# Performance work log

Hardware: AMD Instinct MI355X
Metric: run time of the kernel (lower is better)

The kernel has to match this reference:

```python
import jax, jax.numpy as jnp
import numpy as np

N_HEADS = 16

def _rotate_half(t):
    # t: [B, H, T, hs]; split last dim in half, return cat(-x2, x1)
    hs = t.shape[-1]
    x1, x2 = t[..., : hs // 2], t[..., hs // 2 :]
    return jnp.concatenate((-x2, x1), axis=-1)

def _rope_pos(T, hs, dtype):
    inv_freq = 1.0 / (10000.0 ** (jnp.arange(0, hs, 2, dtype=jnp.float32) / hs))
    freqs = jnp.arange(T, dtype=jnp.float32)[:, None] * inv_freq[None, :]  # [T, hs/2]
    pos = jnp.concatenate((freqs, freqs), axis=-1)  # [T, hs]
    return pos

def setup_inputs() -> dict:
    key = jax.random.key(0)
    ks = jax.random.split(key, 5)
    d = 2048
    x = jax.random.normal(ks[0], (2, 2048, d), dtype=jnp.float32)
    W_attn = jax.random.normal(ks[1], (d, 3 * d), dtype=jnp.float32) * (1.0 / np.sqrt(d))
    b_attn = jax.random.normal(ks[2], (3 * d,), dtype=jnp.float32) * 0.02
    W_proj = jax.random.normal(ks[3], (d, d), dtype=jnp.float32) * (1.0 / np.sqrt(d))
    b_proj = jax.random.normal(ks[4], (d,), dtype=jnp.float32) * 0.02
    return {"x": x, "W_attn": W_attn, "b_attn": b_attn, "W_proj": W_proj, "b_proj": b_proj}

def reference(x, W_attn, b_attn, W_proj, b_proj):
    B, T, C = x.shape
    nh = N_HEADS
    hs = C // nh
    qkv = x @ W_attn + b_attn  # [B, T, 3C]
    q, k, v = jnp.split(qkv, 3, axis=-1)
    # [B, T, C] -> [B, nh, T, hs]
    def to_heads(t):
        return t.reshape(B, T, nh, hs).transpose(0, 2, 1, 3)
    q, k, v = to_heads(q), to_heads(k), to_heads(v)
    # RoPE
    pos = _rope_pos(T, hs, x.dtype)  # [T, hs]
    cos, sin = jnp.cos(pos).astype(x.dtype), jnp.sin(pos).astype(x.dtype)
    q = q * cos + _rotate_half(q) * sin
    k = k * cos + _rotate_half(k) * sin
    # causal SDPA
    scale = 1.0 / np.sqrt(hs)
    scores = jnp.einsum('bhqd,bhkd->bhqk', q, k) * scale  # [B, nh, T, T]
    causal = jnp.tril(jnp.ones((T, T), dtype=bool))
    scores = jnp.where(causal, scores, jnp.finfo(scores.dtype).min)
    att = jax.nn.softmax(scores, axis=-1)
    out = jnp.einsum('bhqk,bhkd->bhqd', att, v)  # [B, nh, T, hs]
    y = out.transpose(0, 2, 1, 3).reshape(B, T, C)
    return y @ W_proj + b_proj
```

## Files before the change

### kernel.cpp

```cpp
#include <hip/hip_runtime.h>
#include <stdint.h>

typedef unsigned short u16;
typedef __attribute__((ext_vector_type(8))) short short8;
typedef __attribute__((ext_vector_type(4))) float f32x4;
typedef __attribute__((ext_vector_type(4))) unsigned short u16x4;

#define DEV __device__ __forceinline__

DEV u16 f2bf(float f) {
  union { float f; unsigned u; } v; v.f = f;
  unsigned r = v.u + 0x7fffu + ((v.u >> 16) & 1u);
  return (u16)(r >> 16);
}
DEV float bf2f(u16 b) {
  union { unsigned u; float f; } v; v.u = ((unsigned)b) << 16;
  return v.f;
}
DEV void gload_lds16(const void* g, void* l) {
  __builtin_amdgcn_global_load_lds((const __attribute__((address_space(1))) void*)g,
                                   (__attribute__((address_space(3))) void*)l,
                                   16, 0, 0);
}
DEV void block_barrier() {
  asm volatile("" ::: "memory");
  __builtin_amdgcn_s_barrier();
  asm volatile("" ::: "memory");
}

__global__ void k_conv(const float* __restrict__ in, u16* __restrict__ out, int n4) {
  int i = blockIdx.x * blockDim.x + threadIdx.x;
  if (i >= n4) return;
  const f32x4 v = *(const f32x4*)(in + (size_t)i * 4);
  u16x4 o;
  o[0] = f2bf(v[0]); o[1] = f2bf(v[1]); o[2] = f2bf(v[2]); o[3] = f2bf(v[3]);
  *(u16x4*)(out + (size_t)i * 4) = o;
}

__global__ void k_tconv(const float* __restrict__ in, u16* __restrict__ out, int R, int C) {
  __shared__ float tile[32][33];
  int c0 = blockIdx.x * 32, r0 = blockIdx.y * 32;
  int tx = threadIdx.x, ty = threadIdx.y;
#pragma unroll
  for (int j = 0; j < 32; j += 8)
    tile[ty + j][tx] = in[(size_t)(r0 + ty + j) * C + (c0 + tx)];
  __syncthreads();
#pragma unroll
  for (int j = 0; j < 32; j += 8)
    out[(size_t)(c0 + ty + j) * R + (r0 + tx)] = f2bf(tile[tx][ty + j]);
}

__global__ void k_rope(const u16* __restrict__ qkv, u16* __restrict__ qh, u16* __restrict__ kh) {
  int m = blockIdx.x;
  int t = m & 2047, b = m >> 11;
  int tid = threadIdx.x;
  int h = blockIdx.y * 4 + (tid >> 6);
  int j = tid & 63;
  float inv = expf((float)j * -0.14391156831212787f);
  float ang = (float)t * inv;
  float s, c;
  sincosf(ang, &s, &c);
  size_t ibase = (size_t)m * 6144 + (size_t)h * 128;
  size_t obase = ((size_t)(b * 16 + h) * 2048 + t) * 128;
  float q1 = bf2f(qkv[ibase + j]),        q2 = bf2f(qkv[ibase + 64 + j]);
  qh[obase + j]      = f2bf(q1 * c - q2 * s);
  qh[obase + 64 + j] = f2bf(q2 * c + q1 * s);
  float k1 = bf2f(qkv[ibase + 2048 + j]), k2 = bf2f(qkv[ibase + 2048 + 64 + j]);
  kh[obase + j]      = f2bf(k1 * c - k2 * s);
  kh[obase + 64 + j] = f2bf(k2 * c + k1 * s);
}

__global__ void k_vtrans(const u16* __restrict__ qkv, u16* __restrict__ vt) {
  __shared__ u16 tile[32][33];
  int bh = blockIdx.z;
  int b = bh >> 4, h = bh & 15;
  int t0 = blockIdx.x * 32, d0 = blockIdx.y * 32;
  int tx = threadIdx.x, ty = threadIdx.y;
#pragma unroll
  for (int j = 0; j < 32; j += 8)
    tile[ty + j][tx] = qkv[(size_t)(b * 2048 + t0 + ty + j) * 6144 + 4096 + h * 128 + d0 + tx];
  __syncthreads();
#pragma unroll
  for (int j = 0; j < 32; j += 8)
    vt[((size_t)bh * 128 + d0 + ty + j) * 2048 + (t0 + tx)] = tile[tx][ty + j];
}

template <bool OUT_BF16>
__global__ __launch_bounds__(256) void k_gemm_tn(const u16* __restrict__ A,
                                                 const u16* __restrict__ Bt,
                                                 const float* __restrict__ bias,
                                                 void* __restrict__ Cv,
                                                 int M, int N, int K) {
  __shared__ __align__(16) short lA[128 * 64];
  __shared__ __align__(16) short lB[128 * 64];
  const int tid = threadIdx.x;
  const int wid = tid >> 6, lane = tid & 63;
  const int bm = blockIdx.x * 128, bn = blockIdx.y * 128;
  const int wm = (wid >> 1) * 64, wn = (wid & 1) * 64;
  const int r = lane & 15, kq = lane >> 4;

  f32x4 acc[4][4];
  const f32x4 zero = {0.f, 0.f, 0.f, 0.f};
#pragma unroll
  for (int i = 0; i < 4; ++i)
#pragma unroll
    for (int j = 0; j < 4; ++j) acc[i][j] = zero;

  for (int k0 = 0; k0 < K; k0 += 64) {
#pragma unroll
    for (int i = 0; i < 4; ++i) {
      int c = (wid * 4 + i) * 64 + lane;
      int row = c >> 3, cb = c & 7;
      gload_lds16(A + (size_t)(bm + row) * K + k0 + cb * 8, (char*)lA + (wid * 4 + i) * 1024);
      gload_lds16(Bt + (size_t)(bn + row) * K + k0 + cb * 8, (char*)lB + (wid * 4 + i) * 1024);
    }
    asm volatile("s_waitcnt vmcnt(0)" ::: "memory");
    __syncthreads();
#pragma unroll
    for (int kk = 0; kk < 2; ++kk) {
      short8 af[4], bfr[4];
#pragma unroll
      for (int mf = 0; mf < 4; ++mf)
        af[mf] = *(const short8*)&lA[(wm + mf * 16 + r) * 64 + kk * 32 + kq * 8];
#pragma unroll
      for (int nf = 0; nf < 4; ++nf)
        bfr[nf] = *(const short8*)&lB[(wn + nf * 16 + r) * 64 + kk * 32 + kq * 8];
#pragma unroll
      for (int mf = 0; mf < 4; ++mf)
#pragma unroll
        for (int nf = 0; nf < 4; ++nf)
          acc[mf][nf] = __builtin_amdgcn_mfma_f32_16x16x32_bf16(af[mf], bfr[nf], acc[mf][nf], 0, 0, 0);
    }
    __syncthreads();
  }
#pragma unroll
  for (int mf = 0; mf < 4; ++mf)
#pragma unroll
    for (int nf = 0; nf < 4; ++nf) {
      int n = bn + wn + nf * 16 + r;
      float bv = bias[n];
#pragma unroll
      for (int i = 0; i < 4; ++i) {
        int m = bm + wm + mf * 16 + kq * 4 + i;
        float val = acc[mf][nf][i] + bv;
        if (OUT_BF16)
          ((u16*)Cv)[(size_t)m * N + n] = f2bf(val);
        else
          ((float*)Cv)[(size_t)m * N + n] = val;
      }
    }
}

__global__ __launch_bounds__(256) void k_attn(const u16* __restrict__ qh,
                                              const u16* __restrict__ kh,
                                              const u16* __restrict__ vt,
                                              u16* __restrict__ out) {
  __shared__ __align__(16) short lK[2][64 * 128];
  __shared__ __align__(16) short lV[2][128 * 64];
  __shared__ __align__(16) short lP[64 * 64];
  const int tid = threadIdx.x, wid = tid >> 6, lane = tid & 63;
  const int p = blockIdx.x, h = blockIdx.y, b = blockIdx.z;
  const size_t bh = (size_t)b * 16 + h;
  const u16* qb = qh + bh * 2048 * 128;
  const u16* kb = kh + bh * 2048 * 128;
  const u16* vb = vt + bh * 128 * 2048;
  const int r = lane & 15, kq = lane >> 4;
  const int r7 = r & 7;
  const int wrow = wid * 16;
  const float scale2 = 0.08838834764831845f * 1.4426950408889634f;

  int koff[4], voff[4];
#pragma unroll
  for (int i = 0; i < 4; ++i) {
    int ci = (wid * 4 + i) * 64 + lane;
    int krow = ci >> 4, kch = ci & 15;
    koff[i] = krow * 128 + ((kch ^ (krow & 7)) * 8);
    int vrow = ci >> 3, vch = ci & 7;
    voff[i] = vrow * 2048 + ((vch ^ (vrow & 7)) * 8);
  }

#pragma unroll 1
  for (int seg = 0; seg < 2; ++seg) {
    const int j = seg ? 31 - p : p;
    const int q0 = j * 64;
    const int nkt = j + 1;

    short8 qa[4];
#pragma unroll
    for (int kk = 0; kk < 4; ++kk)
      qa[kk] = *(const short8*)(qb + (size_t)(q0 + wrow + r) * 128 + kk * 32 + kq * 8);

    f32x4 O[8];
    const f32x4 zero = {0.f, 0.f, 0.f, 0.f};
#pragma unroll
    for (int nf = 0; nf < 8; ++nf) O[nf] = zero;
    float m_run[4], l_run[4];
#pragma unroll
    for (int i = 0; i < 4; ++i) { m_run[i] = -1e30f; l_run[i] = 0.f; }

#pragma unroll
    for (int i = 0; i < 4; ++i) {
      gload_lds16(kb + koff[i], (char*)&lK[0][0] + (wid * 4 + i) * 1024);
      gload_lds16(vb + voff[i], (char*)&lV[0][0] + (wid * 4 + i) * 1024);
    }

#pragma unroll 1
    for (int kt = 0; kt < nkt; ++kt) {
      const int cur = kt & 1;
      if (kt + 1 < nkt) {
        const size_t kbase = (size_t)(kt + 1) * 8192, vbase = (size_t)(kt + 1) * 64;
#pragma unroll
        for (int i = 0; i < 4; ++i) {
          gload_lds16(kb + kbase + koff[i], (char*)&lK[cur ^ 1][0] + (wid * 4 + i) * 1024);
          gload_lds16(vb + vbase + voff[i], (char*)&lV[cur ^ 1][0] + (wid * 4 + i) * 1024);
        }
        asm volatile("s_waitcnt vmcnt(8)" ::: "memory");
      } else {
        asm volatile("s_waitcnt vmcnt(0)" ::: "memory");
      }
      block_barrier();

      f32x4 S[4];
#pragma unroll
      for (int nf = 0; nf < 4; ++nf) S[nf] = zero;
#pragma unroll
      for (int kk = 0; kk < 4; ++kk) {
        short8 kf[4];
#pragma unroll
        for (int nf = 0; nf < 4; ++nf)
          kf[nf] = *(const short8*)&lK[cur][(nf * 16 + r) * 128 + ((kk * 4 + kq) ^ r7) * 8];
#pragma unroll
        for (int nf = 0; nf < 4; ++nf)
          S[nf] = __builtin_amdgcn_mfma_f32_16x16x32_bf16(qa[kk], kf[nf], S[nf], 0, 0, 0);
      }

      float mnew[4];
#pragma unroll
      for (int i = 0; i < 4; ++i) mnew[i] = m_run[i];
      if (kt == nkt - 1) {
#pragma unroll
        for (int nf = 0; nf < 4; ++nf)
#pragma unroll
          for (int i = 0; i < 4; ++i) {
            float s = S[nf][i] * scale2;
            int kg = kt * 64 + nf * 16 + r;
            int qg = q0 + wrow + kq * 4 + i;
            s = (kg > qg) ? -1e30f : s;
            S[nf][i] = s;
            mnew[i] = fmaxf(mnew[i], s);
          }
      } else {
#pragma unroll
        for (int nf = 0; nf < 4; ++nf)
#pragma unroll
          for (int i = 0; i < 4; ++i) {
            float s = S[nf][i] * scale2;
            S[nf][i] = s;
            mnew[i] = fmaxf(mnew[i], s);
          }
      }
#pragma unroll
      for (int i = 0; i < 4; ++i) {
        float v = mnew[i];
        v = fmaxf(v, __shfl_xor(v, 1));
        v = fmaxf(v, __shfl_xor(v, 2));
        v = fmaxf(v, __shfl_xor(v, 4));
        v = fmaxf(v, __shfl_xor(v, 8));
        mnew[i] = v;
      }
      float rs[4];
#pragma unroll
      for (int i = 0; i < 4; ++i) {
        rs[i] = exp2f(m_run[i] - mnew[i]);
        l_run[i] *= rs[i];
        m_run[i] = mnew[i];
      }
#pragma unroll
      for (int nf = 0; nf < 8; ++nf)
#pragma unroll
        for (int i = 0; i < 4; ++i) O[nf][i] *= rs[i];

      {
        float lsum[4] = {0.f, 0.f, 0.f, 0.f};
#pragma unroll
        for (int nf = 0; nf < 4; ++nf)
#pragma unroll
          for (int i = 0; i < 4; ++i) {
            float pv = exp2f(S[nf][i] - m_run[i]);
            lsum[i] += pv;
            int row = wrow + kq * 4 + i;
            int cl = (nf * 2 + (r >> 3)) ^ ((kq * 4 + i) & 7);
            lP[row * 64 + cl * 8 + r7] = (short)f2bf(pv);
          }
#pragma unroll
        for (int i = 0; i < 4; ++i) {
          float v = lsum[i];
          v += __shfl_xor(v, 1);
          v += __shfl_xor(v, 2);
          v += __shfl_xor(v, 4);
          v += __shfl_xor(v, 8);
          l_run[i] += v;
        }
      }

#pragma unroll
      for (int kk = 0; kk < 2; ++kk) {
        short8 pa = *(const short8*)&lP[(wrow + r) * 64 + ((kk * 4 + kq) ^ r7) * 8];
#pragma unroll
        for (int nf = 0; nf < 8; ++nf) {
          short8 vf = *(const short8*)&lV[cur][(nf * 16 + r) * 64 + ((kk * 4 + kq) ^ r7) * 8];
          O[nf] = __builtin_amdgcn_mfma_f32_16x16x32_bf16(pa, vf, O[nf], 0, 0, 0);
        }
      }
      asm volatile("s_waitcnt lgkmcnt(0)" ::: "memory");
      block_barrier();
    }

    float inv[4];
#pragma unroll
    for (int i = 0; i < 4; ++i) inv[i] = 1.f / l_run[i];
#pragma unroll
    for (int nf = 0; nf < 8; ++nf)
#pragma unroll
      for (int i = 0; i < 4; ++i) {
        int qg = q0 + wrow + kq * 4 + i;
        out[(size_t)(b * 2048 + qg) * 2048 + h * 128 + nf * 16 + r] = f2bf(O[nf][i] * inv[i]);
      }
  }
}

extern "C" void kernel_launch(void* const* d_in, const int* in_sizes, int n_in,
                              void* d_out, int out_size, void* d_ws, size_t ws_size,
                              hipStream_t stream) {
  const float* x      = (const float*)d_in[0];
  const float* W_attn = (const float*)d_in[1];
  const float* b_attn = (const float*)d_in[2];
  const float* W_proj = (const float*)d_in[3];
  const float* b_proj = (const float*)d_in[4];
  float* y = (float*)d_out;

  u16* xb     = (u16*)d_ws;
  u16* wqkvT  = xb     + (size_t)4096 * 2048;
  u16* wprojT = wqkvT  + (size_t)6144 * 2048;
  u16* qkv    = wprojT + (size_t)2048 * 2048;
  u16* qh     = qkv    + (size_t)4096 * 6144;
  u16* kh     = qh     + (size_t)4096 * 2048;
  u16* vt     = kh     + (size_t)4096 * 2048;
  u16* attout = vt     + (size_t)4096 * 2048;
  if (ws_size < (size_t)83886080 * 2) return;

  k_conv<<<8192, 256, 0, stream>>>(x, xb, 2097152);
  k_tconv<<<dim3(192, 64), dim3(32, 8), 0, stream>>>(W_attn, wqkvT, 2048, 6144);
  k_tconv<<<dim3(64, 64), dim3(32, 8), 0, stream>>>(W_proj, wprojT, 2048, 2048);
  k_gemm_tn<true><<<dim3(32, 48), 256, 0, stream>>>(xb, wqkvT, b_attn, qkv, 4096, 6144, 2048);
  k_rope<<<dim3(4096, 4), 256, 0, stream>>>(qkv, qh, kh);
  k_vtrans<<<dim3(64, 4, 32), dim3(32, 8), 0, stream>>>(qkv, vt);
  k_attn<<<dim3(16, 16, 2), 256, 0, stream>>>(qh, kh, vt, attout);
  k_gemm_tn<false><<<dim3(32, 16), 256, 0, stream>>>(attout, wprojT, b_proj, y, 4096, 2048, 2048);
}
```

Before: 348.3 us.

## Double-buffer GEMM tiles with XOR-swizzled LDS and 128x256 block tiles

Replaces the single-buffered 128x128 GEMM with a 512-thread 128x256 tile kernel that prefetches the next K-tile into a second LDS buffer while computing the current one. It applies an XOR swizzle to LDS chunk placement to avoid bank conflicts and raises wave priority around the MFMA block. The goal is to hide global-load latency and cut LDS conflicts in both projection GEMMs. It uses 96KB of LDS per block, which limits occupancy, and adds an extra barrier per iteration.

```diff
diff --git a/kernel.cpp b/kernel.cpp
--- a/kernel.cpp
+++ b/kernel.cpp
@@ -86,18 +86,35 @@
 }
 
 template <bool OUT_BF16>
-__global__ __launch_bounds__(256) void k_gemm_tn(const u16* __restrict__ A,
-                                                 const u16* __restrict__ Bt,
-                                                 const float* __restrict__ bias,
-                                                 void* __restrict__ Cv,
-                                                 int M, int N, int K) {
-  __shared__ __align__(16) short lA[128 * 64];
-  __shared__ __align__(16) short lB[128 * 64];
+__global__ __launch_bounds__(512, 2) void k_gemm2(const u16* __restrict__ A,
+                                                  const u16* __restrict__ Bt,
+                                                  const float* __restrict__ bias,
+                                                  void* __restrict__ Cv,
+                                                  int M, int N, int K) {
+  __shared__ __align__(16) short lA[2][128 * 64];
+  __shared__ __align__(16) short lB[2][256 * 64];
   const int tid = threadIdx.x;
   const int wid = tid >> 6, lane = tid & 63;
-  const int bm = blockIdx.x * 128, bn = blockIdx.y * 128;
-  const int wm = (wid >> 1) * 64, wn = (wid & 1) * 64;
-  const int r = lane & 15, kq = lane >> 4;
+  const int bm = blockIdx.x * 128, bn = blockIdx.y * 256;
+  const int wm = (wid >> 2) * 64, wn = (wid & 3) * 64;
+  const int r = lane & 15, kq = lane >> 4, r7 = lane & 7;
+
+  size_t aoff[2]; int albase[2];
+#pragma unroll
+  for (int i = 0; i < 2; ++i) {
+    int c = i * 512 + wid * 64 + lane;
+    int row = c >> 3, ch = c & 7;
+    aoff[i] = (size_t)(bm + row) * K + (ch ^ (row & 7)) * 8;
+    albase[i] = (i * 512 + wid * 64) * 16;
+  }
+  size_t boff[4]; int blbase[4];
+#pragma unroll
+  for (int i = 0; i < 4; ++i) {
+    int c = i * 512 + wid * 64 + lane;
+    int row = c >> 3, ch = c & 7;
+    boff[i] = (size_t)(bn + row) * K + (ch ^ (row & 7)) * 8;
+    blbase[i] = (i * 512 + wid * 64) * 16;
+  }
 
   f32x4 acc[4][4];
   const f32x4 zero = {0.f, 0.f, 0.f, 0.f};
@@ -106,33 +123,65 @@
 #pragma unroll
     for (int j = 0; j < 4; ++j) acc[i][j] = zero;
 
-  for (int k0 = 0; k0 < K; k0 += 64) {
-#pragma unroll
-    for (int i = 0; i < 4; ++i) {
-      int c = (wid * 4 + i) * 64 + lane;
-      int row = c >> 3, cb = c & 7;
-      gload_lds16(A + (size_t)(bm + row) * K + k0 + cb * 8, (char*)lA + (wid * 4 + i) * 1024);
-      gload_lds16(Bt + (size_t)(bn + row) * K + k0 + cb * 8, (char*)lB + (wid * 4 + i) * 1024);
+  const int nt = K >> 6;
+
+#define STAGE_TILE(k0, buf)                                                     \
+  do {                                                                          \
+    _Pragma("unroll")                                                           \
+    for (int i = 0; i < 2; ++i)                                                 \
+      gload_lds16(A + aoff[i] + (k0), (char*)&lA[(buf)][0] + albase[i]);        \
+    _Pragma("unroll")                                                           \
+    for (int i = 0; i < 4; ++i)                                                 \
+      gload_lds16(Bt + boff[i] + (k0), (char*)&lB[(buf)][0] + blbase[i]);       \
+  } while (0)
+
+  STAGE_TILE(0, 0);
+  if (nt > 1) {
+    STAGE_TILE(64, 1);
+    asm volatile("s_waitcnt vmcnt(6)" ::: "memory");
+  } else {
+    asm volatile("s_waitcnt vmcnt(0)" ::: "memory");
+  }
+  block_barrier();
+
+#pragma unroll 1
+  for (int t = 0; t < nt; ++t) {
+    const int cur = t & 1;
+    const short* As = &lA[cur][0];
+    const short* Bs = &lB[cur][0];
+    short8 af[2][4], bfv[2][4];
+#pragma unroll
+    for (int kk = 0; kk < 2; ++kk) {
+#pragma unroll
+      for (int mf = 0; mf < 4; ++mf)
+        af[kk][mf] = *(const short8*)&As[(wm + mf * 16 + r) * 64 + ((kk * 4 + kq) ^ r7) * 8];
+#pragma unroll
+      for (int nf = 0; nf < 4; ++nf)
+        bfv[kk][nf] = *(const short8*)&Bs[(wn + nf * 16 + r) * 64 + ((kk * 4 + kq) ^ r7) * 8];
     }
-    asm volatile("s_waitcnt vmcnt(0)" ::: "memory");
-    __syncthreads();
-#pragma unroll
-    for (int kk = 0; kk < 2; ++kk) {
-      short8 af[4], bfr[4];
+    __builtin_amdgcn_s_setprio(1);
+#pragma unroll
+    for (int kk = 0; kk < 2; ++kk)
 #pragma unroll
       for (int mf = 0; mf < 4; ++mf)
-        af[mf] = *(const short8*)&lA[(wm + mf * 16 + r) * 64 + kk * 32 + kq * 8];
-#pragma unroll
-      for (int nf = 0; nf < 4; ++nf)
-        bfr[nf] = *(const short8*)&lB[(wn + nf * 16 + r) * 64 + kk * 32 + kq * 8];
-#pragma unroll
-      for (int mf = 0; mf < 4; ++mf)
-#pragma unroll
-        for (int nf = 0; nf < 4; ++nf)
-          acc[mf][nf] = __builtin_amdgcn_mfma_f32_16x16x32_bf16(af[mf], bfr[nf], acc[mf][nf], 0, 0, 0);
+#pragma unroll
+        for (int nf = 0; nf < 4; ++nf)
+          acc[mf][nf] = __builtin_amdgcn_mfma_f32_16x16x32_bf16(af[kk][mf], bfv[kk][nf], acc[mf][nf], 0, 0, 0);
+    __builtin_amdgcn_s_setprio(0);
+
+    if (t < nt - 1) {
+      block_barrier();
+      if (t + 2 < nt) {
+        STAGE_TILE((t + 2) * 64, cur);
+        asm volatile("s_waitcnt vmcnt(6)" ::: "memory");
+      } else {
+        asm volatile("s_waitcnt vmcnt(0)" ::: "memory");
+      }
+      block_barrier();
     }
-    __syncthreads();
-  }
+  }
+#undef STAGE_TILE
+
 #pragma unroll
   for (int mf = 0; mf < 4; ++mf)
 #pragma unroll
@@ -352,9 +401,9 @@
   k_conv<<<8192, 256, 0, stream>>>(x, xb, 2097152);
   k_tconv<<<dim3(192, 64), dim3(32, 8), 0, stream>>>(W_attn, wqkvT, 2048, 6144);
   k_tconv<<<dim3(64, 64), dim3(32, 8), 0, stream>>>(W_proj, wprojT, 2048, 2048);
-  k_gemm_tn<true><<<dim3(32, 48), 256, 0, stream>>>(xb, wqkvT, b_attn, qkv, 4096, 6144, 2048);
+  k_gemm2<true><<<dim3(32, 24), 512, 0, stream>>>(xb, wqkvT, b_attn, qkv, 4096, 6144, 2048);
   k_rope<<<dim3(4096, 4), 256, 0, stream>>>(qkv, qh, kh);
   k_vtrans<<<dim3(64, 4, 32), dim3(32, 8), 0, stream>>>(qkv, vt);
   k_attn<<<dim3(16, 16, 2), 256, 0, stream>>>(qh, kh, vt, attout);
-  k_gemm_tn<false><<<dim3(32, 16), 256, 0, stream>>>(attout, wprojT, b_proj, y, 4096, 2048, 2048);
-}
+  k_gemm2<false><<<dim3(32, 8), 512, 0, stream>>>(attout, wprojT, b_proj, y, 4096, 2048, 2048);
+}
```

Result: faster. 332.4 us (-4.6%).

## Replace GEMM with 256x256 double-buffered, swizzled, interleaved-prefetch kernel

Applied to the files above, without the earlier changes.

Both projection GEMMs move from a 128x128 single-buffered tile with full load/wait/compute phases to a 256x256 tile with 8 waves and double-buffered LDS. Global-to-LDS loads for the next K-step are interleaved between MFMA quarter-blocks, and the LDS layout uses an XOR swizzle to avoid bank conflicts. Workgroup IDs are remapped across XCDs and MFMA sections get raised priority. This is meant to hide memory latency and raise MFMA utilisation. The cost is a much smaller grid (128 blocks for the output projection, fewer than the CU count), which risks underusing the GPU, plus 128 KB of LDS per block.

```diff
diff --git a/kernel.cpp b/kernel.cpp
--- a/kernel.cpp
+++ b/kernel.cpp
@@ -86,62 +86,136 @@
 }
 
 template <bool OUT_BF16>
-__global__ __launch_bounds__(256) void k_gemm_tn(const u16* __restrict__ A,
-                                                 const u16* __restrict__ Bt,
-                                                 const float* __restrict__ bias,
-                                                 void* __restrict__ Cv,
-                                                 int M, int N, int K) {
-  __shared__ __align__(16) short lA[128 * 64];
-  __shared__ __align__(16) short lB[128 * 64];
+__global__ __launch_bounds__(512, 2) void k_gemm3(const u16* __restrict__ A,
+                                                  const u16* __restrict__ Bt,
+                                                  const float* __restrict__ bias,
+                                                  void* __restrict__ Cv,
+                                                  int M, int N, int K) {
+  __shared__ __align__(16) short lA[2][256 * 64];
+  __shared__ __align__(16) short lB[2][256 * 64];
   const int tid = threadIdx.x;
   const int wid = tid >> 6, lane = tid & 63;
-  const int bm = blockIdx.x * 128, bn = blockIdx.y * 128;
-  const int wm = (wid >> 1) * 64, wn = (wid & 1) * 64;
-  const int r = lane & 15, kq = lane >> 4;
-
-  f32x4 acc[4][4];
+  const int gx = gridDim.x;
+  const int nwg = gx * gridDim.y;
+  const int orig = blockIdx.y * gx + blockIdx.x;
+  const int lg = (orig & 7) * (nwg >> 3) + (orig >> 3);
+  const int bm = (lg % gx) * 256, bn = (lg / gx) * 256;
+  const int wr = wid >> 2, wc = wid & 3;
+  const int r = lane & 15, kq = lane >> 4, r7 = lane & 7;
+
+  int aoff[4], boff[4], lbase[4];
+#pragma unroll
+  for (int j = 0; j < 4; ++j) {
+    int c = j * 512 + wid * 64 + lane;
+    int row = c >> 3, ch = c & 7;
+    aoff[j] = (bm + row) * K + (ch ^ (row & 7)) * 8;
+    boff[j] = (bn + row) * K + (ch ^ (row & 7)) * 8;
+    lbase[j] = (j * 512 + wid * 64) * 16;
+  }
+
+#define STG_A(k0, buf, j) gload_lds16(A + aoff[j] + (k0), (char*)&lA[(buf)][0] + lbase[j])
+#define STG_B(k0, buf, j) gload_lds16(Bt + boff[j] + (k0), (char*)&lB[(buf)][0] + lbase[j])
+#define RD_A(AF, Q)                                                             \
+  _Pragma("unroll")                                                             \
+  for (int m2 = 0; m2 < 2; ++m2)                                                \
+    _Pragma("unroll")                                                           \
+    for (int kk = 0; kk < 2; ++kk)                                              \
+      AF[m2][kk] = *(const short8*)&As[(wr * 128 + (Q) * 32 + m2 * 16 + r) * 64 \
+                                       + ((kk * 4 + kq) ^ r7) * 8];
+#define QUAD_MFMA(AF, MB)                                                       \
+  __builtin_amdgcn_s_setprio(1);                                                \
+  _Pragma("unroll")                                                             \
+  for (int m2 = 0; m2 < 2; ++m2)                                                \
+    _Pragma("unroll")                                                           \
+    for (int nf = 0; nf < 4; ++nf)                                              \
+      _Pragma("unroll")                                                         \
+      for (int kk = 0; kk < 2; ++kk)                                            \
+        acc[(MB) + m2][nf] = __builtin_amdgcn_mfma_f32_16x16x32_bf16(           \
+            AF[m2][kk], bfr[nf][kk], acc[(MB) + m2][nf], 0, 0, 0);              \
+  __builtin_amdgcn_s_setprio(0);
+
+  f32x4 acc[8][4];
   const f32x4 zero = {0.f, 0.f, 0.f, 0.f};
 #pragma unroll
-  for (int i = 0; i < 4; ++i)
+  for (int i = 0; i < 8; ++i)
 #pragma unroll
     for (int j = 0; j < 4; ++j) acc[i][j] = zero;
 
-  for (int k0 = 0; k0 < K; k0 += 64) {
-#pragma unroll
-    for (int i = 0; i < 4; ++i) {
-      int c = (wid * 4 + i) * 64 + lane;
-      int row = c >> 3, cb = c & 7;
-      gload_lds16(A + (size_t)(bm + row) * K + k0 + cb * 8, (char*)lA + (wid * 4 + i) * 1024);
-      gload_lds16(Bt + (size_t)(bn + row) * K + k0 + cb * 8, (char*)lB + (wid * 4 + i) * 1024);
+  const int nt = K >> 6;
+
+#pragma unroll
+  for (int j = 0; j < 4; ++j) STG_A(0, 0, j);
+#pragma unroll
+  for (int j = 0; j < 4; ++j) STG_B(0, 0, j);
+  if (nt > 1) {
+#pragma unroll
+    for (int j = 0; j < 4; ++j) STG_B(64, 1, j);
+    asm volatile("s_waitcnt vmcnt(4)" ::: "memory");
+  } else {
+    asm volatile("s_waitcnt vmcnt(0)" ::: "memory");
+  }
+  block_barrier();
+
+#pragma unroll 1
+  for (int t = 0; t < nt; ++t) {
+    const int cur = t & 1, nxt = cur ^ 1;
+    const short* As = &lA[cur][0];
+    const short* Bs = &lB[cur][0];
+    const int kA = (t + 1) * 64, kB = (t + 2) * 64;
+    const bool sA = (t + 1 < nt), sB = (t + 2 < nt);
+    short8 bfr[4][2];
+
+#pragma unroll
+    for (int nf = 0; nf < 4; ++nf)
+#pragma unroll
+      for (int kk = 0; kk < 2; ++kk)
+        bfr[nf][kk] = *(const short8*)&Bs[(wc * 64 + nf * 16 + r) * 64 + ((kk * 4 + kq) ^ r7) * 8];
+    short8 af0[2][2];
+    RD_A(af0, 0)
+    if (sA) { STG_A(kA, nxt, 0); STG_A(kA, nxt, 1); }
+    block_barrier();
+    QUAD_MFMA(af0, 0)
+    block_barrier();
+
+    short8 af1[2][2];
+    RD_A(af1, 1)
+    if (sA) { STG_A(kA, nxt, 2); STG_A(kA, nxt, 3); }
+    block_barrier();
+    QUAD_MFMA(af1, 2)
+    block_barrier();
+
+    short8 af2[2][2];
+    RD_A(af2, 2)
+    if (sB) { STG_B(kB, cur, 0); STG_B(kB, cur, 1); }
+    block_barrier();
+    QUAD_MFMA(af2, 4)
+    block_barrier();
+
+    short8 af3[2][2];
+    RD_A(af3, 3)
+    if (sB) { STG_B(kB, cur, 2); STG_B(kB, cur, 3); }
+    block_barrier();
+    QUAD_MFMA(af3, 6)
+    if (t + 1 < nt) {
+      if (sB) asm volatile("s_waitcnt vmcnt(4)" ::: "memory");
+      else    asm volatile("s_waitcnt vmcnt(0)" ::: "memory");
     }
-    asm volatile("s_waitcnt vmcnt(0)" ::: "memory");
-    __syncthreads();
-#pragma unroll
-    for (int kk = 0; kk < 2; ++kk) {
-      short8 af[4], bfr[4];
-#pragma unroll
-      for (int mf = 0; mf < 4; ++mf)
-        af[mf] = *(const short8*)&lA[(wm + mf * 16 + r) * 64 + kk * 32 + kq * 8];
-#pragma unroll
-      for (int nf = 0; nf < 4; ++nf)
-        bfr[nf] = *(const short8*)&lB[(wn + nf * 16 + r) * 64 + kk * 32 + kq * 8];
-#pragma unroll
-      for (int mf = 0; mf < 4; ++mf)
-#pragma unroll
-        for (int nf = 0; nf < 4; ++nf)
-          acc[mf][nf] = __builtin_amdgcn_mfma_f32_16x16x32_bf16(af[mf], bfr[nf], acc[mf][nf], 0, 0, 0);
-    }
-    __syncthreads();
+    block_barrier();
   }
-#pragma unroll
-  for (int mf = 0; mf < 4; ++mf)
+#undef STG_A
+#undef STG_B
+#undef RD_A
+#undef QUAD_MFMA
+
+#pragma unroll
+  for (int mf = 0; mf < 8; ++mf)
 #pragma unroll
     for (int nf = 0; nf < 4; ++nf) {
-      int n = bn + wn + nf * 16 + r;
+      int n = bn + wc * 64 + nf * 16 + r;
       float bv = bias[n];
 #pragma unroll
       for (int i = 0; i < 4; ++i) {
-        int m = bm + wm + mf * 16 + kq * 4 + i;
+        int m = bm + wr * 128 + mf * 16 + kq * 4 + i;
         float val = acc[mf][nf][i] + bv;
         if (OUT_BF16)
           ((u16*)Cv)[(size_t)m * N + n] = f2bf(val);
@@ -352,9 +426,9 @@
   k_conv<<<8192, 256, 0, stream>>>(x, xb, 2097152);
   k_tconv<<<dim3(192, 64), dim3(32, 8), 0, stream>>>(W_attn, wqkvT, 2048, 6144);
   k_tconv<<<dim3(64, 64), dim3(32, 8), 0, stream>>>(W_proj, wprojT, 2048, 2048);
-  k_gemm_tn<true><<<dim3(32, 48), 256, 0, stream>>>(xb, wqkvT, b_attn, qkv, 4096, 6144, 2048);
+  k_gemm3<true><<<dim3(16, 24), 512, 0, stream>>>(xb, wqkvT, b_attn, qkv, 4096, 6144, 2048);
   k_rope<<<dim3(4096, 4), 256, 0, stream>>>(qkv, qh, kh);
   k_vtrans<<<dim3(64, 4, 32), dim3(32, 8), 0, stream>>>(qkv, vt);
   k_attn<<<dim3(16, 16, 2), 256, 0, stream>>>(qh, kh, vt, attout);
-  k_gemm_tn<false><<<dim3(32, 16), 256, 0, stream>>>(attout, wprojT, b_proj, y, 4096, 2048, 2048);
-}
+  k_gemm3<false><<<dim3(16, 8), 512, 0, stream>>>(attout, wprojT, b_proj, y, 4096, 2048, 2048);
+}
```

Result: faster. 335.4 us (-3.7%).
